# Optimization experiments

Hardware: AMD Instinct MI355X
Metric: run time of the kernel (lower is better)

Reference implementation:

```python
import jax, jax.numpy as jnp
import numpy as np

ALPHA = 1.0
BETA = 1.0
# interval_quality lookup table indexed by |m - h| % 12
# 0:1.0 1:0.5 2:0.3 3:0.2 4:0.1 5:0.1 6:0.7 7:0.0 8:0.2 9:0.3 10:0.4 11:0.5
QUALITY = jnp.array([1.0, 0.5, 0.3, 0.2, 0.1, 0.1, 0.7, 0.0, 0.2, 0.3, 0.4, 0.5], dtype=jnp.float32)

def setup_inputs() -> dict:
    key = jax.random.key(0)
    k1, k2, k3 = jax.random.split(key, 3)
    B, T, V = 64, 2048, 128
    outputs = jax.random.normal(k1, (B, T, V), dtype=jnp.float32)
    targets = jax.random.normal(k2, (B, T, V), dtype=jnp.float32)
    melodies = jax.random.normal(k3, (B, T, V), dtype=jnp.float32)
    return {"outputs": outputs, "targets": targets, "melodies": melodies}

def reference(outputs, targets, melodies):
    # MSE over all elements
    mse_loss = jnp.mean((outputs - targets) ** 2)
    # vectorized argmax over pitch dim -> [B, T] int indices
    melody_note = jnp.argmax(melodies, axis=-1)
    harmony_note = jnp.argmax(outputs, axis=-1)
    interval = jnp.abs(melody_note - harmony_note) % 12
    harmony_loss = jnp.mean(QUALITY[interval])
    return ALPHA * mse_loss + BETA * harmony_loss
```

## Files before the change

kernel.cpp:

```cpp
#include <hip/hip_runtime.h>

#define NROWS (64 * 2048)
#define VDIM  128
#define NELEM (16777216.0f)

__constant__ float c_quality[12] = {1.0f, 0.5f, 0.3f, 0.2f, 0.1f, 0.1f,
                                    0.7f, 0.0f, 0.2f, 0.3f, 0.4f, 0.5f};

__global__ __launch_bounds__(256) void mtl_kernel(const float* __restrict__ outputs,
                                                  const float* __restrict__ targets,
                                                  const float* __restrict__ melodies,
                                                  float* __restrict__ out) {
    const int tid  = threadIdx.x;
    const int lane = tid & 63;
    const int wid  = tid >> 6;
    const int gw   = blockIdx.x * 4 + wid;
    const int GW   = gridDim.x * 4;
    const int half = lane >> 5;
    const int l32  = lane & 31;

    float msum = 0.0f;
    float hsum = 0.0f;

    for (int rp = gw; rp < NROWS / 2; rp += GW) {
        const int row = rp * 2 + half;
        const float4* op = reinterpret_cast<const float4*>(outputs  + (size_t)row * VDIM);
        const float4* tp = reinterpret_cast<const float4*>(targets  + (size_t)row * VDIM);
        const float4* mp = reinterpret_cast<const float4*>(melodies + (size_t)row * VDIM);
        float4 o = op[l32];
        float4 t = tp[l32];
        float4 m = mp[l32];

        float dx = o.x - t.x, dy = o.y - t.y, dz = o.z - t.z, dw = o.w - t.w;
        msum = fmaf(dx, dx, msum);
        msum = fmaf(dy, dy, msum);
        msum = fmaf(dz, dz, msum);
        msum = fmaf(dw, dw, msum);

        float ov = o.x; int oi = 0;
        if (o.y > ov) { ov = o.y; oi = 1; }
        if (o.z > ov) { ov = o.z; oi = 2; }
        if (o.w > ov) { ov = o.w; oi = 3; }
        oi += l32 * 4;
        float mv = m.x; int mi = 0;
        if (m.y > mv) { mv = m.y; mi = 1; }
        if (m.z > mv) { mv = m.z; mi = 2; }
        if (m.w > mv) { mv = m.w; mi = 3; }
        mi += l32 * 4;

        #pragma unroll
        for (int off = 16; off >= 1; off >>= 1) {
            float ov2 = __shfl_xor(ov, off);
            int   oi2 = __shfl_xor(oi, off);
            if (ov2 > ov || (ov2 == ov && oi2 < oi)) { ov = ov2; oi = oi2; }
            float mv2 = __shfl_xor(mv, off);
            int   mi2 = __shfl_xor(mi, off);
            if (mv2 > mv || (mv2 == mv && mi2 < mi)) { mv = mv2; mi = mi2; }
        }

        if (l32 == 0) {
            int d = mi - oi;
            if (d < 0) d = -d;
            hsum += c_quality[d % 12];
        }
    }

    #pragma unroll
    for (int off = 32; off >= 1; off >>= 1) {
        msum += __shfl_xor(msum, off);
        hsum += __shfl_xor(hsum, off);
    }

    __shared__ float s_m[4];
    __shared__ float s_h[4];
    if (lane == 0) { s_m[wid] = msum; s_h[wid] = hsum; }
    __syncthreads();

    if (tid == 0) {
        float mt = s_m[0] + s_m[1] + s_m[2] + s_m[3];
        float ht = s_h[0] + s_h[1] + s_h[2] + s_h[3];
        float contrib = mt * (1.0f / NELEM) + ht * (1.0f / (float)NROWS);
        atomicAdd(out, contrib);
    }
}

extern "C" void kernel_launch(void* const* d_in, const int* in_sizes, int n_in,
                              void* d_out, int out_size, void* d_ws, size_t ws_size,
                              hipStream_t stream) {
    const float* outputs  = (const float*)d_in[0];
    const float* targets  = (const float*)d_in[1];
    const float* melodies = (const float*)d_in[2];
    float* out = (float*)d_out;

    hipMemsetAsync(out, 0, sizeof(float), stream);

    const int blocks = 2048;
    mtl_kernel<<<blocks, 256, 0, stream>>>(outputs, targets, melodies, out);
}
```

Baseline: 59.94 us.

## Prefetch next rows and use packed-key DPP argmax reduction

The row loop now has a compile-time trip count, is fully unrolled, and loads the next iteration's float4 values before computing on the current ones, so more memory traffic is in flight. Argmax now packs each candidate's order-preserving float key and its index into one 32-bit word and reduces it with DPP row ops plus a single shuffle. This replaces the paired value and index shuffles. The constant-memory quality table becomes a bit-packed immediate, and every lane accumulates the harmony term, with the scale factor adjusted to match. The packed key drops the low 7 bits of the float, so near-ties may resolve differently from an exact argmax, and the fixed loop count assumes the grid exactly divides the rows.

```diff
diff --git a/kernel.cpp b/kernel.cpp
--- a/kernel.cpp
+++ b/kernel.cpp
@@ -1,35 +1,73 @@
 #include <hip/hip_runtime.h>
 
-#define NROWS (64 * 2048)
-#define VDIM  128
-#define NELEM (16777216.0f)
+#define BLOCKS 2048
+#define TPB    256
+#define WAVES  (BLOCKS * (TPB / 64))
+#define NROWS  (64 * 2048)
+#define PAIRS  (NROWS / 2)
+#define ITERS  (PAIRS / WAVES)
+#define VDIM   128
+#define NELEM  16777216.0f
 
-__constant__ float c_quality[12] = {1.0f, 0.5f, 0.3f, 0.2f, 0.1f, 0.1f,
-                                    0.7f, 0.0f, 0.2f, 0.3f, 0.4f, 0.5f};
+#define QTAB 0x54320711235AULL
 
-__global__ __launch_bounds__(256) void mtl_kernel(const float* __restrict__ outputs,
+__device__ __forceinline__ unsigned int fkey(float f) {
+    unsigned int u = __float_as_uint(f);
+    unsigned int m = ((unsigned int)((int)u >> 31)) | 0x80000000u;
+    return u ^ m;
+}
+
+__device__ __forceinline__ unsigned int rowmax16(unsigned int k) {
+    unsigned int t;
+    t = (unsigned int)__builtin_amdgcn_update_dpp(0, (int)k, 0x121, 0xF, 0xF, true);
+    k = k > t ? k : t;
+    t = (unsigned int)__builtin_amdgcn_update_dpp(0, (int)k, 0x122, 0xF, 0xF, true);
+    k = k > t ? k : t;
+    t = (unsigned int)__builtin_amdgcn_update_dpp(0, (int)k, 0x124, 0xF, 0xF, true);
+    k = k > t ? k : t;
+    t = (unsigned int)__builtin_amdgcn_update_dpp(0, (int)k, 0x128, 0xF, 0xF, true);
+    k = k > t ? k : t;
+    return k;
+}
+
+__device__ __forceinline__ unsigned int lane_key(float4 v, int l32) {
+    float bv = v.x; int bi = 0;
+    if (v.y > bv) { bv = v.y; bi = 1; }
+    if (v.z > bv) { bv = v.z; bi = 2; }
+    if (v.w > bv) { bv = v.w; bi = 3; }
+    int idx = l32 * 4 + bi;
+    return (fkey(bv) & 0xFFFFFF80u) | (unsigned int)(127 - idx);
+}
+
+__global__ __launch_bounds__(TPB) void mtl_kernel(const float* __restrict__ outputs,
                                                   const float* __restrict__ targets,
                                                   const float* __restrict__ melodies,
                                                   float* __restrict__ out) {
     const int tid  = threadIdx.x;
     const int lane = tid & 63;
     const int wid  = tid >> 6;
-    const int gw   = blockIdx.x * 4 + wid;
-    const int GW   = gridDim.x * 4;
+    const int gw   = blockIdx.x * (TPB / 64) + wid;
     const int half = lane >> 5;
     const int l32  = lane & 31;
+
+    const size_t base = (size_t)(2 * gw + half) * (VDIM / 4) + l32;
+    const float4* __restrict__ ob = reinterpret_cast<const float4*>(outputs)  + base;
+    const float4* __restrict__ tb = reinterpret_cast<const float4*>(targets)  + base;
+    const float4* __restrict__ mb = reinterpret_cast<const float4*>(melodies) + base;
+    const size_t step = (size_t)WAVES * 2 * (VDIM / 4);
 
     float msum = 0.0f;
     float hsum = 0.0f;
 
-    for (int rp = gw; rp < NROWS / 2; rp += GW) {
-        const int row = rp * 2 + half;
-        const float4* op = reinterpret_cast<const float4*>(outputs  + (size_t)row * VDIM);
-        const float4* tp = reinterpret_cast<const float4*>(targets  + (size_t)row * VDIM);
-        const float4* mp = reinterpret_cast<const float4*>(melodies + (size_t)row * VDIM);
-        float4 o = op[l32];
-        float4 t = tp[l32];
-        float4 m = mp[l32];
+    float4 o = ob[0], t = tb[0], m = mb[0];
+
+    #pragma unroll
+    for (int it = 0; it < ITERS; ++it) {
+        float4 on = o, tn = t, mn = m;
+        if (it + 1 < ITERS) {
+            size_t noff = (size_t)(it + 1) * step;
+            on = ob[noff]; tn = tb[noff]; mn = mb[noff];
+        }
 
         float dx = o.x - t.x, dy = o.y - t.y, dz = o.z - t.z, dw = o.w - t.w;
         msum = fmaf(dx, dx, msum);
@@ -37,32 +75,24 @@
         msum = fmaf(dz, dz, msum);
         msum = fmaf(dw, dw, msum);
 
-        float ov = o.x; int oi = 0;
-        if (o.y > ov) { ov = o.y; oi = 1; }
-        if (o.z > ov) { ov = o.z; oi = 2; }
-        if (o.w > ov) { ov = o.w; oi = 3; }
-        oi += l32 * 4;
-        float mv = m.x; int mi = 0;
-        if (m.y > mv) { mv = m.y; mi = 1; }
-        if (m.z > mv) { mv = m.z; mi = 2; }
-        if (m.w > mv) { mv = m.w; mi = 3; }
-        mi += l32 * 4;
+        unsigned int ok = lane_key(o, l32);
+        unsigned int mk = lane_key(m, l32);
+        ok = rowmax16(ok);
+        mk = rowmax16(mk);
+        unsigned int ok2 = (unsigned int)__shfl_xor((int)ok, 16);
+        unsigned int mk2 = (unsigned int)__shfl_xor((int)mk, 16);
+        ok = ok > ok2 ? ok : ok2;
+        mk = mk > mk2 ? mk : mk2;
 
-        #pragma unroll
-        for (int off = 16; off >= 1; off >>= 1) {
-            float ov2 = __shfl_xor(ov, off);
-            int   oi2 = __shfl_xor(oi, off);
-            if (ov2 > ov || (ov2 == ov && oi2 < oi)) { ov = ov2; oi = oi2; }
-            float mv2 = __shfl_xor(mv, off);
-            int   mi2 = __shfl_xor(mi, off);
-            if (mv2 > mv || (mv2 == mv && mi2 < mi)) { mv = mv2; mi = mi2; }
-        }
+        int oi = 127 - (int)(ok & 127u);
+        int mi = 127 - (int)(mk & 127u);
+        int d = mi - oi;
+        if (d < 0) d = -d;
+        int interval = d % 12;
+        float q = (float)((unsigned int)(QTAB >> (interval << 2)) & 15u) * 0.1f;
+        hsum += q;
 
-        if (l32 == 0) {
-            int d = mi - oi;
-            if (d < 0) d = -d;
-            hsum += c_quality[d % 12];
-        }
+        o = on; t = tn; m = mn;
     }
 
     #pragma unroll
@@ -71,15 +101,15 @@
         hsum += __shfl_xor(hsum, off);
     }
 
-    __shared__ float s_m[4];
-    __shared__ float s_h[4];
+    __shared__ float s_m[TPB / 64];
+    __shared__ float s_h[TPB / 64];
     if (lane == 0) { s_m[wid] = msum; s_h[wid] = hsum; }
     __syncthreads();
 
     if (tid == 0) {
         float mt = s_m[0] + s_m[1] + s_m[2] + s_m[3];
         float ht = s_h[0] + s_h[1] + s_h[2] + s_h[3];
-        float contrib = mt * (1.0f / NELEM) + ht * (1.0f / (float)NROWS);
+        float contrib = mt * (1.0f / NELEM) + ht * (1.0f / 4194304.0f);
         atomicAdd(out, contrib);
     }
 }
@@ -93,7 +123,5 @@
     float* out = (float*)d_out;
 
     hipMemsetAsync(out, 0, sizeof(float), stream);
-
-    const int blocks = 2048;
-    mtl_kernel<<<blocks, 256, 0, stream>>>(outputs, targets, melodies, out);
+    mtl_kernel<<<BLOCKS, TPB, 0, stream>>>(outputs, targets, melodies, out);
 }
```

After: 51.31 us. 14.4% less time.
